# Optimization experiments

Measured on AMD Instinct MI355X. Metric: run time of the kernel, lower is better.

The kernel has to match this reference:

```python
import jax, jax.numpy as jnp
import numpy as np

B, N, C, H = 4, 2048, 1024, 16
D = C // H
SCALE = D ** -0.5


def setup_inputs() -> dict:
    key = jax.random.key(0)
    k1, k2, k3 = jax.random.split(key, 3)
    x = jax.random.normal(k1, (B, N, C), dtype=jnp.float32)
    w_qkv = jax.random.normal(k2, (C, 3 * C), dtype=jnp.float32) * (C ** -0.5)
    w_proj = jax.random.normal(k3, (C, C), dtype=jnp.float32) * (C ** -0.5)
    b_proj = jnp.zeros((C,), dtype=jnp.float32)
    return {"x": x, "w_qkv": w_qkv, "w_proj": w_proj, "b_proj": b_proj}


def reference(x, w_qkv, w_proj, b_proj):
    # qkv projection (no bias): [B,N,3C] -> [3,B,H,N,D]
    qkv = (x @ w_qkv).reshape(B, N, 3, H, D).transpose(2, 0, 3, 1, 4)
    q, k, v = qkv[0], qkv[1], qkv[2]
    # scores [B,H,N,N]
    attn = jax.nn.softmax(jnp.einsum('bhnd,bhmd->bhnm', q, k) * SCALE, axis=-1)
    out = jnp.einsum('bhnm,bhmd->bhnd', attn, v)          # [B,H,N,D]
    out = out.transpose(0, 2, 1, 3).reshape(B, N, C)       # [B,N,C]
    return out @ w_proj + b_proj
```

## Files before the change

kernel.cpp:

```cpp
#include <hip/hip_runtime.h>
#include <hip/hip_bf16.h>
#include <cstdint>
#include <cstddef>

typedef unsigned int uint;
typedef unsigned short ushort;

constexpr int Bn = 4, Nn = 2048, Cc = 1024, Hh = 16;
constexpr int ROWS = Bn * Nn;
constexpr int QKVC = 3 * Cc;
constexpr float SL2 = 0.18033688011118f;

typedef __bf16 bf16_t;
typedef bf16_t bf16x8 __attribute__((ext_vector_type(8)));
typedef float f32x4 __attribute__((ext_vector_type(4)));

__device__ __forceinline__ ushort f2bf(float f) {
  union { __bf16 b; ushort u; } cv;
  cv.b = (__bf16)f;
  return cv.u;
}
__device__ __forceinline__ float exp2v(float x) { return __builtin_exp2f(x); }

__device__ __forceinline__ void gload_lds16(const void* g, void* l) {
  __builtin_amdgcn_global_load_lds(
      (const __attribute__((address_space(1))) void*)g,
      (__attribute__((address_space(3))) void*)l, 16, 0, 0);
}

__global__ __launch_bounds__(256) void cvt_bf16_kernel(
    const float* __restrict__ in, ushort* __restrict__ out) {
  int i = blockIdx.x * 256 + threadIdx.x;
  const float4* ip = (const float4*)in;
  float4 a = ip[i * 2], b = ip[i * 2 + 1];
  uint4 w;
  w.x = (uint)f2bf(a.x) | ((uint)f2bf(a.y) << 16);
  w.y = (uint)f2bf(a.z) | ((uint)f2bf(a.w) << 16);
  w.z = (uint)f2bf(b.x) | ((uint)f2bf(b.y) << 16);
  w.w = (uint)f2bf(b.z) | ((uint)f2bf(b.w) << 16);
  ((uint4*)out)[i] = w;
}

__global__ __launch_bounds__(256) void transpose_cvt_kernel(
    const float* __restrict__ W, ushort* __restrict__ Wt, int K, int N) {
  __shared__ float tile[64][65];
  const int n0 = blockIdx.x * 64, k0 = blockIdx.y * 64;
  const int tid = threadIdx.x;
#pragma unroll
  for (int it = 0; it < 16; it++) {
    int idx = tid + it * 256;
    int r = idx >> 6, c = idx & 63;
    tile[r][c] = W[(size_t)(k0 + r) * N + n0 + c];
  }
  __syncthreads();
#pragma unroll
  for (int it = 0; it < 16; it++) {
    int idx = tid + it * 256;
    int r = idx >> 6, c = idx & 63;
    Wt[(size_t)(n0 + r) * K + k0 + c] = f2bf(tile[c][r]);
  }
}

template <int MODE>
__global__ __launch_bounds__(256) void gemm128_kernel(
    const ushort* __restrict__ A, const ushort* __restrict__ Bt,
    void* __restrict__ Cout, void* __restrict__ Vout,
    const float* __restrict__ bias, int M, int N, int K) {
  __shared__ ushort As[128 * 64];
  __shared__ ushort Bs[128 * 64];
  const int tid = threadIdx.x;
  const int lane = tid & 63;
  const int wid = tid >> 6;
  const int wm = wid >> 1, wn = wid & 1;
  const int l16 = lane & 15, g = lane >> 4;
  const int n0 = blockIdx.x * 128, m0 = blockIdx.y * 128;

  const ushort* Ab = A + (size_t)m0 * K;
  const ushort* Bb = Bt + (size_t)n0 * K;
  f32x4 acc[4][4] = {};

  int srow[4], scol[4];
#pragma unroll
  for (int i = 0; i < 4; i++) {
    int c = tid + i * 256;
    srow[i] = c >> 3;
    scol[i] = ((c & 7) ^ (srow[i] & 7)) * 8;
  }

  for (int k0 = 0; k0 < K; k0 += 64) {
#pragma unroll
    for (int i = 0; i < 4; i++) {
      int c = tid + i * 256;
      gload_lds16(Ab + (size_t)srow[i] * K + k0 + scol[i], As + c * 8);
      gload_lds16(Bb + (size_t)srow[i] * K + k0 + scol[i], Bs + c * 8);
    }
    __syncthreads();
#pragma unroll
    for (int kc = 0; kc < 2; kc++) {
      bf16x8 af[4], bfr[4];
#pragma unroll
      for (int mf = 0; mf < 4; mf++) {
        int row = wm * 64 + mf * 16 + l16;
        af[mf] = *(const bf16x8*)(As + row * 64 + (((kc * 4 + g) ^ (row & 7)) * 8));
      }
#pragma unroll
      for (int nf = 0; nf < 4; nf++) {
        int row = wn * 64 + nf * 16 + l16;
        bfr[nf] = *(const bf16x8*)(Bs + row * 64 + (((kc * 4 + g) ^ (row & 7)) * 8));
      }
#pragma unroll
      for (int mf = 0; mf < 4; mf++)
#pragma unroll
        for (int nf = 0; nf < 4; nf++)
          acc[mf][nf] = __builtin_amdgcn_mfma_f32_16x16x32_bf16(af[mf], bfr[nf], acc[mf][nf], 0, 0, 0);
    }
    __syncthreads();
  }

#pragma unroll
  for (int mf = 0; mf < 4; mf++) {
    const int orow0 = m0 + wm * 64 + mf * 16 + g * 4;
#pragma unroll
    for (int nf = 0; nf < 4; nf++) {
      int col = n0 + wn * 64 + nf * 16 + l16;
      if (MODE == 0) {
        if (col < 2048) {
          const float qs = (col < 1024) ? SL2 : 1.0f;
#pragma unroll
          for (int r = 0; r < 4; r++)
            ((ushort*)Cout)[(size_t)(orow0 + r) * 2048 + col] = f2bf(acc[mf][nf][r] * qs);
        } else {
          int hh = (col - 2048) >> 6, dd = (col - 2048) & 63;
          int bb = orow0 >> 11, nn = orow0 & 2047;
          ushort4 w;
          w.x = f2bf(acc[mf][nf][0]); w.y = f2bf(acc[mf][nf][1]);
          w.z = f2bf(acc[mf][nf][2]); w.w = f2bf(acc[mf][nf][3]);
          *(ushort4*)((ushort*)Vout + ((size_t)(bb * 16 + hh) * 64 + dd) * 2048 + nn) = w;
        }
      } else {
#pragma unroll
        for (int r = 0; r < 4; r++)
          ((float*)Cout)[(size_t)(orow0 + r) * N + col] = acc[mf][nf][r] + bias[col];
      }
    }
  }
}

__global__ __launch_bounds__(256, 4) void flash_mfma_kernel(
    const ushort* __restrict__ qk, const ushort* __restrict__ vt,
    ushort* __restrict__ obf) {
  __shared__ ushort Ks[2][64 * 64];
  __shared__ ushort Vs[2][64 * 64];
  const int tid = threadIdx.x;
  const int lane = tid & 63, wid = tid >> 6;
  const int l16 = lane & 15, g = lane >> 4;

  const int f = blockIdx.x + (int)(gridDim.x * blockIdx.y);
  const int xcd = f & 7, slot = f >> 3;
  const int bh = xcd * 8 + (slot >> 4);
  const int qx = slot & 15;
  const int b = bh >> 4, h = bh & 15;
  const int q0 = qx * 128 + wid * 32;

  const int sc0 = tid, sc1 = tid + 256;
  const int sr0 = sc0 >> 3, scol0 = ((sc0 & 7) ^ (sr0 & 7)) * 8;
  const int sr1 = sc1 >> 3, scol1 = ((sc1 & 7) ^ (sr1 & 7)) * 8;
  const ushort* Kbase = qk + (size_t)b * Nn * 2048 + 1024 + h * 64;
  const ushort* Vbase = vt + (size_t)bh * 64 * 2048;

#define STAGE(buf, kv0)                                                       \
  do {                                                                        \
    gload_lds16(Kbase + (size_t)((kv0) + sr0) * 2048 + scol0,                 \
                &Ks[buf][0] + sc0 * 8);                                       \
    gload_lds16(Kbase + (size_t)((kv0) + sr1) * 2048 + scol1,                 \
                &Ks[buf][0] + sc1 * 8);                                       \
    gload_lds16(Vbase + (size_t)sr0 * 2048 + (kv0) + scol0,                   \
                &Vs[buf][0] + sc0 * 8);                                       \
    gload_lds16(Vbase + (size_t)sr1 * 2048 + (kv0) + scol1,                   \
                &Vs[buf][0] + sc1 * 8);                                       \
  } while (0)

  bf16x8 qf[2][2];
#pragma unroll
  for (int qh = 0; qh < 2; qh++)
#pragma unroll
    for (int kc = 0; kc < 2; kc++)
      qf[qh][kc] = *(const bf16x8*)(
          qk + (size_t)(b * Nn + q0 + qh * 16 + l16) * 2048 + h * 64 + kc * 32 + g * 8);

  union { ushort us[8]; bf16x8 v; } onesu;
#pragma unroll
  for (int j = 0; j < 8; j++) onesu.us[j] = 0x3F80;
  const bf16x8 ones = onesu.v;

  f32x4 oacc[2][4] = {};
  f32x4 lacc[2] = {};

  STAGE(0, 0);

  for (int t = 0; t < Nn / 64; ++t) {
    const int cur = t & 1;
    asm volatile("s_waitcnt vmcnt(0)" ::: "memory");
    __builtin_amdgcn_s_barrier();
    asm volatile("" ::: "memory");
    if (t < Nn / 64 - 1) STAGE(cur ^ 1, (t + 1) * 64);

    const ushort* Kc = &Ks[cur][0];
    const ushort* Vc = &Vs[cur][0];

    f32x4 sacc[2][4] = {};
    __builtin_amdgcn_s_setprio(1);
#pragma unroll
    for (int kc = 0; kc < 2; kc++) {
#pragma unroll
      for (int jc = 0; jc < 4; jc++) {
        int row = jc * 16 + l16;
        bf16x8 kf = *(const bf16x8*)(Kc + row * 64 + ((kc * 32 + g * 8) ^ ((row & 7) << 3)));
        sacc[0][jc] = __builtin_amdgcn_mfma_f32_16x16x32_bf16(kf, qf[0][kc], sacc[0][jc], 0, 0, 0);
        sacc[1][jc] = __builtin_amdgcn_mfma_f32_16x16x32_bf16(kf, qf[1][kc], sacc[1][jc], 0, 0, 0);
      }
    }
    __builtin_amdgcn_s_setprio(0);

    bf16x8 pa[2][2];
#pragma unroll
    for (int qh = 0; qh < 2; qh++) {
      uint pk_[4][2];
#pragma unroll
      for (int jc = 0; jc < 4; jc++) {
        float p0 = exp2v(sacc[qh][jc][0]);
        float p1 = exp2v(sacc[qh][jc][1]);
        float p2 = exp2v(sacc[qh][jc][2]);
        float p3 = exp2v(sacc[qh][jc][3]);
        asm("v_cvt_pk_bf16_f32 %0, %1, %2" : "=v"(pk_[jc][0]) : "v"(p0), "v"(p1));
        asm("v_cvt_pk_bf16_f32 %0, %1, %2" : "=v"(pk_[jc][1]) : "v"(p2), "v"(p3));
      }
#pragma unroll
      for (int kc = 0; kc < 2; kc++) {
        uint a0 = pk_[kc * 2][0], b0 = pk_[kc * 2 + 1][0];
        asm("v_permlane32_swap_b32 %0, %1" : "+v"(a0), "+v"(b0));
        asm("v_permlane16_swap_b32 %0, %1" : "+v"(a0), "+v"(b0));
        uint a1 = pk_[kc * 2][1], b1 = pk_[kc * 2 + 1][1];
        asm("v_permlane32_swap_b32 %0, %1" : "+v"(a1), "+v"(b1));
        asm("v_permlane16_swap_b32 %0, %1" : "+v"(a1), "+v"(b1));
        union { uint4 u; bf16x8 v; } cv;
        cv.u.x = a0; cv.u.y = a1; cv.u.z = b0; cv.u.w = b1;
        pa[qh][kc] = cv.v;
      }
    }

    __builtin_amdgcn_s_setprio(1);
#pragma unroll
    for (int kc = 0; kc < 2; kc++) {
#pragma unroll
      for (int dc = 0; dc < 4; dc++) {
        int row = dc * 16 + l16;
        bf16x8 vf = *(const bf16x8*)(Vc + row * 64 + ((kc * 32 + g * 8) ^ ((row & 7) << 3)));
        oacc[0][dc] = __builtin_amdgcn_mfma_f32_16x16x32_bf16(pa[0][kc], vf, oacc[0][dc], 0, 0, 0);
        oacc[1][dc] = __builtin_amdgcn_mfma_f32_16x16x32_bf16(pa[1][kc], vf, oacc[1][dc], 0, 0, 0);
      }
      lacc[0] = __builtin_amdgcn_mfma_f32_16x16x32_bf16(pa[0][kc], ones, lacc[0], 0, 0, 0);
      lacc[1] = __builtin_amdgcn_mfma_f32_16x16x32_bf16(pa[1][kc], ones, lacc[1], 0, 0, 0);
    }
    __builtin_amdgcn_s_setprio(0);
  }
#undef STAGE

#pragma unroll
  for (int qh = 0; qh < 2; qh++) {
    f32x4 linv;
#pragma unroll
    for (int r = 0; r < 4; r++) linv[r] = 1.f / lacc[qh][r];
#pragma unroll
    for (int r = 0; r < 4; r++) {
      int grow = b * Nn + q0 + qh * 16 + g * 4 + r;
      ushort* op = obf + (size_t)grow * Cc + h * 64 + l16;
#pragma unroll
      for (int dc = 0; dc < 4; dc++)
        op[dc * 16] = f2bf(oacc[qh][dc][r] * linv[r]);
    }
  }
}

extern "C" void kernel_launch(void* const* d_in, const int* in_sizes, int n_in,
                              void* d_out, int out_size, void* d_ws, size_t ws_size,
                              hipStream_t stream) {
  const float* x      = (const float*)d_in[0];
  const float* w_qkv  = (const float*)d_in[1];
  const float* w_proj = (const float*)d_in[2];
  const float* b_proj = (const float*)d_in[3];
  float* out = (float*)d_out;

  char* ws = (char*)d_ws;
  ushort* Xbf    = (ushort*)(ws);
  ushort* WqkvT  = (ushort*)(ws + (16u << 20));
  ushort* WprojT = (ushort*)(ws + (22u << 20));
  ushort* QKbf   = (ushort*)(ws + (24u << 20));
  ushort* Vtg    = (ushort*)(ws + (56u << 20));
  ushort* Obf    = (ushort*)(ws + (72u << 20));

  cvt_bf16_kernel<<<4096, 256, 0, stream>>>(x, Xbf);
  transpose_cvt_kernel<<<dim3(QKVC / 64, Cc / 64), 256, 0, stream>>>(w_qkv, WqkvT, Cc, QKVC);
  transpose_cvt_kernel<<<dim3(Cc / 64, Cc / 64), 256, 0, stream>>>(w_proj, WprojT, Cc, Cc);
  gemm128_kernel<0><<<dim3(QKVC / 128, ROWS / 128), 256, 0, stream>>>(
      Xbf, WqkvT, QKbf, Vtg, nullptr, ROWS, QKVC, Cc);
  flash_mfma_kernel<<<dim3(Nn / 128, Bn * Hh), 256, 0, stream>>>(QKbf, Vtg, Obf);
  gemm128_kernel<1><<<dim3(Cc / 128, ROWS / 128), 256, 0, stream>>>(
      Obf, WprojT, out, nullptr, b_proj, ROWS, Cc, Cc);
}
```

Before: 209.0 us.

## Merge prep kernels into one launch and remap GEMM blocks per XCD

Folds the x-to-bf16 conversion and the two weight transpose-conversions into a single prep kernel that picks its role by block index, which removes two kernel launches and their gaps. It also changes the GEMM block index mapping so that consecutive blocks, which the hardware spreads round-robin across the 8 XCDs, get M-tiles grouped per XCD. The intent is better L2 reuse of the A rows within each XCD. The cost is some extra integer arithmetic per block and a branch in the prep kernel.

After: 203.9 us (median of 2 runs). 2.5% less time.

```diff
diff --git a/kernel.cpp b/kernel.cpp
--- a/kernel.cpp
+++ b/kernel.cpp
@@ -28,24 +28,33 @@
       (__attribute__((address_space(3))) void*)l, 16, 0, 0);
 }
 
-__global__ __launch_bounds__(256) void cvt_bf16_kernel(
-    const float* __restrict__ in, ushort* __restrict__ out) {
-  int i = blockIdx.x * 256 + threadIdx.x;
-  const float4* ip = (const float4*)in;
-  float4 a = ip[i * 2], b = ip[i * 2 + 1];
-  uint4 w;
-  w.x = (uint)f2bf(a.x) | ((uint)f2bf(a.y) << 16);
-  w.y = (uint)f2bf(a.z) | ((uint)f2bf(a.w) << 16);
-  w.z = (uint)f2bf(b.x) | ((uint)f2bf(b.y) << 16);
-  w.w = (uint)f2bf(b.z) | ((uint)f2bf(b.w) << 16);
-  ((uint4*)out)[i] = w;
-}
-
-__global__ __launch_bounds__(256) void transpose_cvt_kernel(
-    const float* __restrict__ W, ushort* __restrict__ Wt, int K, int N) {
+__global__ __launch_bounds__(256) void prep_kernel(
+    const float* __restrict__ x, ushort* __restrict__ xbf,
+    const float* __restrict__ wqkv, ushort* __restrict__ wqkvt,
+    const float* __restrict__ wproj, ushort* __restrict__ wprojt) {
   __shared__ float tile[64][65];
-  const int n0 = blockIdx.x * 64, k0 = blockIdx.y * 64;
+  const int blk = blockIdx.x;
   const int tid = threadIdx.x;
+  if (blk < 4096) {
+    int i = blk * 256 + tid;
+    const float4* ip = (const float4*)x;
+    float4 a = ip[i * 2], b = ip[i * 2 + 1];
+    uint4 w;
+    w.x = (uint)f2bf(a.x) | ((uint)f2bf(a.y) << 16);
+    w.y = (uint)f2bf(a.z) | ((uint)f2bf(a.w) << 16);
+    w.z = (uint)f2bf(b.x) | ((uint)f2bf(b.y) << 16);
+    w.w = (uint)f2bf(b.z) | ((uint)f2bf(b.w) << 16);
+    ((uint4*)xbf)[i] = w;
+    return;
+  }
+  const float* W;
+  ushort* Wt;
+  int N, bx;
+  if (blk < 4096 + 768) { W = wqkv; Wt = wqkvt; N = QKVC; bx = blk - 4096; }
+  else                  { W = wproj; Wt = wprojt; N = Cc; bx = blk - 4864; }
+  const int K = Cc;
+  const int nb = N >> 6;
+  const int n0 = (bx % nb) * 64, k0 = (bx / nb) * 64;
 #pragma unroll
   for (int it = 0; it < 16; it++) {
     int idx = tid + it * 256;
@@ -73,7 +82,13 @@
   const int wid = tid >> 6;
   const int wm = wid >> 1, wn = wid & 1;
   const int l16 = lane & 15, g = lane >> 4;
-  const int n0 = blockIdx.x * 128, m0 = blockIdx.y * 128;
+
+  const int nx = gridDim.x;
+  const int f = blockIdx.x + (int)(nx * blockIdx.y);
+  const int xcd = f & 7, s = f >> 3;
+  const int by = xcd * ((int)gridDim.y >> 3) + s / nx;
+  const int bx = s % nx;
+  const int n0 = bx * 128, m0 = by * 128;
 
   const ushort* Ab = A + (size_t)m0 * K;
   const ushort* Bb = Bt + (size_t)n0 * K;
@@ -299,9 +314,7 @@
   ushort* Vtg    = (ushort*)(ws + (56u << 20));
   ushort* Obf    = (ushort*)(ws + (72u << 20));
 
-  cvt_bf16_kernel<<<4096, 256, 0, stream>>>(x, Xbf);
-  transpose_cvt_kernel<<<dim3(QKVC / 64, Cc / 64), 256, 0, stream>>>(w_qkv, WqkvT, Cc, QKVC);
-  transpose_cvt_kernel<<<dim3(Cc / 64, Cc / 64), 256, 0, stream>>>(w_proj, WprojT, Cc, Cc);
+  prep_kernel<<<5120, 256, 0, stream>>>(x, Xbf, w_qkv, WqkvT, w_proj, WprojT);
   gemm128_kernel<0><<<dim3(QKVC / 128, ROWS / 128), 256, 0, stream>>>(
       Xbf, WqkvT, QKbf, Vtg, nullptr, ROWS, QKVC, Cc);
   flash_mfma_kernel<<<dim3(Nn / 128, Bn * Hh), 256, 0, stream>>>(QKbf, Vtg, Obf);
```
